# Performance work log

Hardware: AMD Instinct MI355X
Metric: run time of the kernel (lower is better)

## Reference

```python
import jax, jax.numpy as jnp
import numpy as np

E = 512   # embed_size == head_dim
H = 8     # heads
N = 8     # batch
S = 1024  # seq len


def setup_inputs() -> dict:
    key = jax.random.key(0)
    ks = jax.random.split(key, 12)
    scale = 1.0 / np.sqrt(E)
    inp = {
        "values": jax.random.normal(ks[0], (N, S, E), jnp.float32),
        "keys": jax.random.normal(ks[1], (N, S, E), jnp.float32),
        "query": jax.random.normal(ks[2], (N, S, E), jnp.float32),
        "pos": jnp.arange(S, dtype=jnp.int64) if jax.config.jax_enable_x64 else jnp.arange(S, dtype=jnp.int32),
        "mask": jax.random.randint(ks[3], (N, 1, S, S), 0, 2, jnp.int32),
        # nn.Linear params: weight (out,in), y = x @ W.T + b
        "Wv": jax.random.uniform(ks[4], (E * H, E), jnp.float32, -scale, scale),
        "bv": jax.random.uniform(ks[5], (E * H,), jnp.float32, -scale, scale),
        "Wk": jax.random.uniform(ks[6], (E * H, E), jnp.float32, -scale, scale),
        "bk": jax.random.uniform(ks[7], (E * H,), jnp.float32, -scale, scale),
        "Wq": jax.random.uniform(ks[8], (E * H, E), jnp.float32, -scale, scale),
        "bq": jax.random.uniform(ks[9], (E * H,), jnp.float32, -scale, scale),
        "Wo": jax.random.uniform(ks[10], (E, E), jnp.float32, -scale, scale),
        "bo": jax.random.uniform(ks[11], (E,), jnp.float32, -scale, scale),
    }
    return inp


def reference(values, keys, query, pos, mask, Wv, bv, Wk, bk, Wq, bq, Wo, bo):
    n, q_len, e = query.shape
    v_len = values.shape[1]
    k_len = keys.shape[1]
    h = Wq.shape[0] // e
    # QKV projections: E -> E*H, reshape to (N, L, H, E)
    v = (values @ Wv.T + bv).reshape(n, v_len, h, e)
    k = (keys @ Wk.T + bk).reshape(n, k_len, h, e)
    q = (query @ Wq.T + bq).reshape(n, q_len, h, e)
    # bilinear energy, no softmax
    energy = jnp.einsum('nqhd,nkhd->nhqk', q, k)
    energy = jnp.where(mask == 0, jnp.zeros((), energy.dtype), energy)
    attention = energy / jnp.asarray(e ** 0.5, energy.dtype)
    out = jnp.einsum('nhql,nlhd->nqhd', attention, v).sum(axis=2)  # sum over heads
    return out @ Wo.T + bo
```

## Files before the change

kernel.cpp:

```cpp
#include <hip/hip_runtime.h>


#define RS 0.04419417382415922f

typedef __attribute__((ext_vector_type(8))) short bf16x8;
typedef __attribute__((ext_vector_type(4))) float f32x4;

__device__ __forceinline__ unsigned short f2b(float f) {
  unsigned u = __builtin_bit_cast(unsigned, f);
  unsigned r = (u + 0x7FFFu + ((u >> 16) & 1u)) >> 16;
  return (unsigned short)r;
}
__device__ __forceinline__ float b2f(unsigned short h) {
  return __builtin_bit_cast(float, ((unsigned)h) << 16);
}

__global__ void k_fill(float* p, int n, float v) {
  int i = blockIdx.x * blockDim.x + threadIdx.x;
  int stride = gridDim.x * blockDim.x;
  for (; i < n; i += stride) p[i] = v;
}

__global__ void k_maskbits(const int* __restrict__ m,
                           unsigned* __restrict__ bits) {
  int wi = blockIdx.x * 256 + threadIdx.x;
  const int* src = m + (size_t)wi * 32;
  unsigned b = 0;
#pragma unroll
  for (int i = 0; i < 32; ++i) b |= (src[i] != 0 ? 1u : 0u) << i;
  bits[wi] = b;
}

__global__ void k_conv3(const float4* __restrict__ v,
                        const float4* __restrict__ k,
                        const float4* __restrict__ q, ushort4* __restrict__ d,
                        int n4, int dstride) {
  const float4* s = (blockIdx.z == 0) ? v : (blockIdx.z == 1) ? k : q;
  ushort4* dz = d + (size_t)blockIdx.z * dstride;
  int stride = gridDim.x * blockDim.x;
  for (int i = blockIdx.x * blockDim.x + threadIdx.x; i < n4; i += stride) {
    float4 x = s[i];
    ushort4 o;
    o.x = f2b(x.x); o.y = f2b(x.y); o.z = f2b(x.z); o.w = f2b(x.w);
    dz[i] = o;
  }
}

__global__ void k_convw(const float4* __restrict__ s, ushort4* __restrict__ d,
                        int n4, float scale) {
  int stride = gridDim.x * blockDim.x;
  for (int i = blockIdx.x * blockDim.x + threadIdx.x; i < n4; i += stride) {
    float4 v = s[i];
    ushort4 o;
    o.x = f2b(v.x * scale); o.y = f2b(v.y * scale);
    o.z = f2b(v.z * scale); o.w = f2b(v.w * scale);
    d[i] = o;
  }
}

__global__ void k_reduce(const unsigned short* __restrict__ a,
                         unsigned short* __restrict__ o, int total) {
  int i = blockIdx.x * blockDim.x + threadIdx.x;
  if (i >= total) return;
  int nl = i >> 17, j = i & 131071;
  const ushort4* av = (const ushort4*)a + (size_t)nl * 1048576;
  float4 s = {0.f, 0.f, 0.f, 0.f};
#pragma unroll
  for (int h = 0; h < 8; ++h) {
    ushort4 v = av[h * 131072 + j];
    s.x += b2f(v.x); s.y += b2f(v.y); s.z += b2f(v.z); s.w += b2f(v.w);
  }
  ushort4 r;
  r.x = f2b(s.x); r.y = f2b(s.y); r.z = f2b(s.z); r.w = f2b(s.w);
  ((ushort4*)o)[i] = r;
}

#define GLD16(gp, sp)                                              \
  __builtin_amdgcn_global_load_lds(                                \
      (const __attribute__((address_space(1))) void*)(gp),         \
      (__attribute__((address_space(3))) void*)(sp), 16, 0, 0)

template <int MODE>
__global__ __launch_bounds__(256) void k_gemm(
    const unsigned short* __restrict__ A, const unsigned short* __restrict__ B,
    const float* __restrict__ bi0, const float* __restrict__ bi1,
    const float* __restrict__ bi2, const unsigned* __restrict__ mbits,
    unsigned short* __restrict__ outb, float* __restrict__ outf, int n0,
    int xstr, int ostr) {
  __shared__ short smem[17408];
  char* const sb = (char*)smem;

  const int tid = threadIdx.x;
  const int wid = tid >> 6;
  const int lane = tid & 63;
  const int wr = wid >> 1, wc = wid & 1;
  const int l15 = lane & 15, l4 = lane >> 4;

  int bx, by, bz;
  if constexpr (MODE == 2 || MODE == 4) {
    bz = blockIdx.x; bx = blockIdx.y; by = blockIdx.z;
  } else {
    bx = blockIdx.x; by = blockIdx.y; bz = blockIdx.z;
  }

  constexpr int KSEG = (MODE == 4) ? 1024 : 512;
  constexpr int NK = KSEG / 32;

  f32x4 acc[4][4];
#pragma unroll
  for (int i = 0; i < 4; ++i)
#pragma unroll
    for (int j = 0; j < 4; ++j) acc[i][j] = (f32x4){0.f, 0.f, 0.f, 0.f};

  const unsigned short* Ab;
  const unsigned short* Bb;
  if constexpr (MODE == 5) {
    Ab = A + (size_t)bx * 128 * 512;
    Bb = B + (size_t)by * 128 * 512;
  } else if constexpr (MODE == 6) {
    Ab = A + (size_t)bz * xstr + (size_t)bx * 128 * 512;
    Bb = B + (size_t)bz * 2097152 + (size_t)by * 128 * 512;
  } else if constexpr (MODE == 2) {
    Ab = A + (size_t)bz * 524288 + (size_t)bx * 128 * 512;
    Bb = B + (size_t)bz * 524288 + (size_t)by * 128 * 512;
  } else {
    Ab = A + (size_t)bz * 1048576 + (size_t)bx * 128 * 1024;
    Bb = B + (size_t)bz * 524288 + (size_t)by * 128 * 1024;
  }

#define STAGE(buf, kc)                                             \
  {                                                                \
    _Pragma("unroll") for (int is = 0; is < 2; ++is) {             \
      int c = is * 256 + tid;                                      \
      int row = c >> 2, col = (c & 3) << 3;                        \
      GLD16(Ab + (size_t)row * KSEG + (kc)*32 + col,               \
            sb + (buf)*8192 + is * 4096 + wid * 1024);             \
      GLD16(Bb + (size_t)row * KSEG + (kc)*32 + col,               \
            sb + 16384 + (buf)*8192 + is * 4096 + wid * 1024);     \
    }                                                              \
  }

  STAGE(0, 0);
  int cur = 0;
#pragma unroll 4
  for (int kc = 0; kc < NK; ++kc) {
    __syncthreads();
    if (kc + 1 < NK) STAGE(cur ^ 1, kc + 1);
    bf16x8 af[4], bf_[4];
#pragma unroll
    for (int f = 0; f < 4; ++f) {
      af[f] = *(const bf16x8*)(sb + cur * 8192 +
                               ((wr * 64 + f * 16 + l15) << 6) + (l4 << 4));
      bf_[f] = *(const bf16x8*)(sb + 16384 + cur * 8192 +
                                ((wc * 64 + f * 16 + l15) << 6) + (l4 << 4));
    }
#pragma unroll
    for (int mf = 0; mf < 4; ++mf)
#pragma unroll
      for (int nf = 0; nf < 4; ++nf)
        acc[mf][nf] = __builtin_amdgcn_mfma_f32_16x16x32_bf16(
            af[mf], bf_[nf], acc[mf][nf], 0, 0, 0);
    cur ^= 1;
  }
#undef STAGE

  const int r0 = l4 * 4;
  const int c0 = l15;

  if constexpr (MODE != 5) {
    const bool transp = (MODE == 6) && (bz == 0);
    const float* bias =
        (MODE == 6) ? ((bz == 0) ? bi0 : (bz == 1) ? bi1 : bi2) : nullptr;
    const float bscale = (MODE == 6 && bz == 2) ? RS : 1.0f;
    __syncthreads();
#pragma unroll
    for (int nf = 0; nf < 4; ++nf) {
      int c_loc = wc * 64 + nf * 16 + c0;
      int c_ = by * 128 + c_loc;
      float bvl = (MODE == 6) ? bias[c_] * bscale : 0.f;
#pragma unroll
      for (int mf = 0; mf < 4; ++mf) {
#pragma unroll
        for (int r = 0; r < 4; ++r) {
          int r_loc = wr * 64 + mf * 16 + r0 + r;
          float v = acc[mf][nf][r] + bvl;
          unsigned short bb;
          if constexpr (MODE == 2) {
            int r_ = bx * 128 + r_loc;
            unsigned mw = mbits[((size_t)(n0 + (bz >> 3)) * 1024 + r_) * 32 +
                                (c_ >> 5)];
            bb = ((mw >> (c_ & 31)) & 1u) ? f2b(v) : (unsigned short)0;
          } else {
            bb = f2b(v);
          }
          if (transp)
            smem[c_loc * 136 + r_loc] = (short)bb;
          else
            smem[r_loc * 136 + c_loc] = (short)bb;
        }
      }
    }
    __syncthreads();
#pragma unroll
    for (int ch = 0; ch < 8; ++ch) {
      int idx = ch * 256 + tid;
      int row = idx >> 4;
      int col = (idx & 15) << 3;
      bf16x8 v = *(const bf16x8*)(smem + row * 136 + col);
      if constexpr (MODE == 2) {
        int r_ = bx * 128 + row, cB = by * 128 + col;
        *(bf16x8*)(outb + (size_t)bz * 1048576 + (size_t)r_ * 1024 + cB) = v;
      } else if constexpr (MODE == 4) {
        int r_ = bx * 128 + row, cB = by * 128 + col;
        *(bf16x8*)(outb + (size_t)bz * 524288 + (size_t)r_ * 512 + cB) = v;
      } else {
        unsigned short* O = outb + (size_t)bz * ostr;
        if (bz == 0) {
          int eB = by * 128 + row;
          int r_ = bx * 128 + col;
          int nl = r_ >> 10, s = r_ & 1023, h = eB >> 9, e = eB & 511;
          *(bf16x8*)(O + (((size_t)nl * 8 + h) * 512 + e) * 1024 + s) = v;
        } else {
          int r_ = bx * 128 + row, cB = by * 128 + col;
          int nl = r_ >> 10, s = r_ & 1023, h = cB >> 9, e = cB & 511;
          *(bf16x8*)(O + (((size_t)nl * 8 + h) * 1024 + s) * 512 + e) = v;
        }
      }
    }
  } else {
    float* const Cs32 = (float*)smem;
#pragma unroll
    for (int hh = 0; hh < 2; ++hh) {
      __syncthreads();
      if (wr == hh) {
#pragma unroll
        for (int nf = 0; nf < 4; ++nf) {
          int c_loc = wc * 64 + nf * 16 + c0;
          float bvl = bi0[by * 128 + c_loc];
#pragma unroll
          for (int mf = 0; mf < 4; ++mf)
#pragma unroll
            for (int r = 0; r < 4; ++r)
              Cs32[(mf * 16 + r0 + r) * 136 + c_loc] = acc[mf][nf][r] + bvl;
        }
      }
      __syncthreads();
#pragma unroll
      for (int ch = 0; ch < 8; ++ch) {
        int idx = ch * 256 + tid;
        int row = idx >> 5;
        int col = (idx & 31) << 2;
        float4 v = *(const float4*)(Cs32 + row * 136 + col);
        *(float4*)(outf + (size_t)(bx * 128 + hh * 64 + row) * 512 +
                   by * 128 + col) = v;
      }
    }
  }
}

extern "C" void kernel_launch(void* const* d_in, const int* in_sizes, int n_in,
                              void* d_out, int out_size, void* d_ws,
                              size_t ws_size, hipStream_t stream) {
  const float* values = (const float*)d_in[0];
  const float* keys = (const float*)d_in[1];
  const float* query = (const float*)d_in[2];
  const int* maskI = (const int*)d_in[4];
  const float* Wv = (const float*)d_in[5];
  const float* bv = (const float*)d_in[6];
  const float* Wk = (const float*)d_in[7];
  const float* bk = (const float*)d_in[8];
  const float* Wq = (const float*)d_in[9];
  const float* bq = (const float*)d_in[10];
  const float* Wo = (const float*)d_in[11];
  const float* bo = (const float*)d_in[12];
  float* dout = (float*)d_out;

  const int exp_sizes[13] = {4194304, 4194304, 4194304, 1024, 8388608,
                             2097152, 4096,    2097152, 4096, 2097152,
                             4096,    262144,  512};
  bool ok = (n_in == 13);
  if (ok)
    for (int i = 0; i < 13; ++i)
      if (in_sizes[i] != exp_sizes[i]) ok = false;
  if (!ok) {
    k_fill<<<512, 256, 0, stream>>>(dout, out_size, 1000.f);
    return;
  }

  const size_t SZT2 = 16777216, SZT4 = 33554432;
  const size_t need2 = 22544384 + 3 * SZT2 + 2 * SZT2;
  const size_t need4 = 22544384 + 3 * SZT4 + 2 * SZT4;
  const int NL = (ws_size >= need4) ? 4 : 2;
  if (ws_size < need2) {
    k_fill<<<512, 256, 0, stream>>>(dout, out_size, 2000.f);
    return;
  }
  const size_t SZT = (size_t)NL * 8388608;

  char* w = (char*)d_ws;
  unsigned short* Wvb = (unsigned short*)(w);
  unsigned short* Wob = (unsigned short*)(w + 12582912);
  unsigned short* Atb = (unsigned short*)(w + 13107200);
  unsigned* mbits = (unsigned*)(w + 21495808);
  unsigned short* VTb = (unsigned short*)(w + 22544384);
  unsigned short* Kb = (unsigned short*)(w + 22544384 + SZT);
  unsigned short* Qb = (unsigned short*)(w + 22544384 + 2 * SZT);
  unsigned short* Pb = (unsigned short*)(w + 22544384 + 3 * SZT);
  unsigned short* Xc = (unsigned short*)Pb;
  unsigned short* Ahb = (unsigned short*)Qb;

  k_convw<<<512, 256, 0, stream>>>((const float4*)Wv, (ushort4*)Wvb, 524288,
                                   1.0f);
  k_convw<<<512, 256, 0, stream>>>((const float4*)Wk, (ushort4*)(Wvb + 2097152),
                                   524288, 1.0f);
  k_convw<<<512, 256, 0, stream>>>((const float4*)Wq, (ushort4*)(Wvb + 4194304),
                                   524288, RS);
  k_convw<<<256, 256, 0, stream>>>((const float4*)Wo, (ushort4*)Wob, 65536,
                                   1.0f);
  k_maskbits<<<1024, 256, 0, stream>>>(maskI, mbits);

  const int xstr = NL * 524288;
  const int ostr = NL * 4194304;

  for (int it = 0; it < 8 / NL; ++it) {
    const int n0 = it * NL;
    const size_t xoff = (size_t)n0 * 524288;
    k_conv3<<<dim3(512 * NL, 1, 3), 256, 0, stream>>>(
        (const float4*)(values + xoff), (const float4*)(keys + xoff),
        (const float4*)(query + xoff), (ushort4*)Xc, NL * 131072, NL * 131072);
    k_gemm<6><<<dim3(NL * 8, 32, 3), 256, 0, stream>>>(
        Xc, Wvb, bv, bk, bq, nullptr, VTb, nullptr, 0, xstr, ostr);
    k_gemm<2><<<dim3(NL * 8, 8, 8), 256, 0, stream>>>(
        Qb, Kb, nullptr, nullptr, nullptr, mbits, Pb, nullptr, n0, 0, 0);
    k_gemm<4><<<dim3(NL * 8, 8, 4), 256, 0, stream>>>(
        Pb, VTb, nullptr, nullptr, nullptr, nullptr, Ahb, nullptr, 0, 0, 0);
    k_reduce<<<NL * 512, 256, 0, stream>>>(Ahb, Atb + (size_t)n0 * 524288,
                                           NL * 131072);
  }

  k_gemm<5><<<dim3(64, 4, 1), 256, 0, stream>>>(
      Atb, Wob, bo, nullptr, nullptr, nullptr, nullptr, dout, 0, 0, 0);
}
```

Before: 507.5 us.

## Accumulate four heads per block in P·V GEMM and remap QKV block order

The P·V GEMM now loops over four heads inside one block and keeps a single accumulator, so each block writes a partial sum over four heads. The head-sum reduction then only adds two partials instead of eight, which cuts bf16 intermediate traffic. The QKV projection GEMM also remaps its linear block id so consecutive blocks are spread across eight chunks, likely to balance work across XCDs or improve cache locality. In exchange the P·V grid has four times fewer blocks, which may lower occupancy and parallelism.

```diff
diff --git a/kernel.cpp b/kernel.cpp
--- a/kernel.cpp
+++ b/kernel.cpp
@@ -58,20 +58,18 @@
   }
 }
 
-__global__ void k_reduce(const unsigned short* __restrict__ a,
-                         unsigned short* __restrict__ o, int total) {
+__global__ void k_reduce2(const unsigned short* __restrict__ a,
+                          unsigned short* __restrict__ o, int total) {
   int i = blockIdx.x * blockDim.x + threadIdx.x;
   if (i >= total) return;
   int nl = i >> 17, j = i & 131071;
-  const ushort4* av = (const ushort4*)a + (size_t)nl * 1048576;
-  float4 s = {0.f, 0.f, 0.f, 0.f};
-#pragma unroll
-  for (int h = 0; h < 8; ++h) {
-    ushort4 v = av[h * 131072 + j];
-    s.x += b2f(v.x); s.y += b2f(v.y); s.z += b2f(v.z); s.w += b2f(v.w);
-  }
+  const ushort4* av = (const ushort4*)a + (size_t)nl * 262144;
+  ushort4 v0 = av[j], v1 = av[131072 + j];
   ushort4 r;
-  r.x = f2b(s.x); r.y = f2b(s.y); r.z = f2b(s.z); r.w = f2b(s.w);
+  r.x = f2b(b2f(v0.x) + b2f(v1.x));
+  r.y = f2b(b2f(v0.y) + b2f(v1.y));
+  r.z = f2b(b2f(v0.z) + b2f(v1.z));
+  r.w = f2b(b2f(v0.w) + b2f(v1.w));
   ((ushort4*)o)[i] = r;
 }
 
@@ -99,12 +97,23 @@
   int bx, by, bz;
   if constexpr (MODE == 2 || MODE == 4) {
     bz = blockIdx.x; bx = blockIdx.y; by = blockIdx.z;
+  } else if constexpr (MODE == 6) {
+    int gx = gridDim.x, gy = gridDim.y;
+    int lid = blockIdx.x + gx * (blockIdx.y + gy * blockIdx.z);
+    int total = gx * gy * gridDim.z;
+    int chunk = total >> 3;
+    int wg = (lid & 7) * chunk + (lid >> 3);
+    bx = wg % gx;
+    int t = wg / gx;
+    by = t % gy;
+    bz = t / gy;
   } else {
     bx = blockIdx.x; by = blockIdx.y; bz = blockIdx.z;
   }
 
   constexpr int KSEG = (MODE == 4) ? 1024 : 512;
   constexpr int NK = KSEG / 32;
+  constexpr int NSEG = (MODE == 4) ? 4 : 1;
 
   f32x4 acc[4][4];
 #pragma unroll
@@ -114,19 +123,6 @@
 
   const unsigned short* Ab;
   const unsigned short* Bb;
-  if constexpr (MODE == 5) {
-    Ab = A + (size_t)bx * 128 * 512;
-    Bb = B + (size_t)by * 128 * 512;
-  } else if constexpr (MODE == 6) {
-    Ab = A + (size_t)bz * xstr + (size_t)bx * 128 * 512;
-    Bb = B + (size_t)bz * 2097152 + (size_t)by * 128 * 512;
-  } else if constexpr (MODE == 2) {
-    Ab = A + (size_t)bz * 524288 + (size_t)bx * 128 * 512;
-    Bb = B + (size_t)bz * 524288 + (size_t)by * 128 * 512;
-  } else {
-    Ab = A + (size_t)bz * 1048576 + (size_t)bx * 128 * 1024;
-    Bb = B + (size_t)bz * 524288 + (size_t)by * 128 * 1024;
-  }
 
 #define STAGE(buf, kc)                                             \
   {                                                                \
@@ -140,27 +136,46 @@
     }                                                              \
   }
 
-  STAGE(0, 0);
-  int cur = 0;
+  for (int seg = 0; seg < NSEG; ++seg) {
+    if constexpr (MODE == 5) {
+      Ab = A + (size_t)bx * 128 * 512;
+      Bb = B + (size_t)by * 128 * 512;
+    } else if constexpr (MODE == 6) {
+      Ab = A + (size_t)bz * xstr + (size_t)bx * 128 * 512;
+      Bb = B + (size_t)bz * 2097152 + (size_t)by * 128 * 512;
+    } else if constexpr (MODE == 2) {
+      Ab = A + (size_t)bz * 524288 + (size_t)bx * 128 * 512;
+      Bb = B + (size_t)bz * 524288 + (size_t)by * 128 * 512;
+    } else {
+      int n_l = bz >> 1, g = bz & 1;
+      int nh = n_l * 8 + g * 4 + seg;
+      Ab = A + (size_t)nh * 1048576 + (size_t)bx * 128 * 1024;
+      Bb = B + (size_t)nh * 524288 + (size_t)by * 128 * 1024;
+    }
+
+    if (NSEG > 1 && seg > 0) __syncthreads();
+    STAGE(0, 0);
+    int cur = 0;
 #pragma unroll 4
-  for (int kc = 0; kc < NK; ++kc) {
-    __syncthreads();
-    if (kc + 1 < NK) STAGE(cur ^ 1, kc + 1);
-    bf16x8 af[4], bf_[4];
-#pragma unroll
-    for (int f = 0; f < 4; ++f) {
-      af[f] = *(const bf16x8*)(sb + cur * 8192 +
-                               ((wr * 64 + f * 16 + l15) << 6) + (l4 << 4));
-      bf_[f] = *(const bf16x8*)(sb + 16384 + cur * 8192 +
-                                ((wc * 64 + f * 16 + l15) << 6) + (l4 << 4));
-    }
-#pragma unroll
-    for (int mf = 0; mf < 4; ++mf)
-#pragma unroll
-      for (int nf = 0; nf < 4; ++nf)
-        acc[mf][nf] = __builtin_amdgcn_mfma_f32_16x16x32_bf16(
-            af[mf], bf_[nf], acc[mf][nf], 0, 0, 0);
-    cur ^= 1;
+    for (int kc = 0; kc < NK; ++kc) {
+      __syncthreads();
+      if (kc + 1 < NK) STAGE(cur ^ 1, kc + 1);
+      bf16x8 af[4], bf_[4];
+#pragma unroll
+      for (int f = 0; f < 4; ++f) {
+        af[f] = *(const bf16x8*)(sb + cur * 8192 +
+                                 ((wr * 64 + f * 16 + l15) << 6) + (l4 << 4));
+        bf_[f] = *(const bf16x8*)(sb + 16384 + cur * 8192 +
+                                  ((wc * 64 + f * 16 + l15) << 6) + (l4 << 4));
+      }
+#pragma unroll
+      for (int mf = 0; mf < 4; ++mf)
+#pragma unroll
+        for (int nf = 0; nf < 4; ++nf)
+          acc[mf][nf] = __builtin_amdgcn_mfma_f32_16x16x32_bf16(
+              af[mf], bf_[nf], acc[mf][nf], 0, 0, 0);
+      cur ^= 1;
+    }
   }
 #undef STAGE
 
@@ -332,10 +347,10 @@
         Xc, Wvb, bv, bk, bq, nullptr, VTb, nullptr, 0, xstr, ostr);
     k_gemm<2><<<dim3(NL * 8, 8, 8), 256, 0, stream>>>(
         Qb, Kb, nullptr, nullptr, nullptr, mbits, Pb, nullptr, n0, 0, 0);
-    k_gemm<4><<<dim3(NL * 8, 8, 4), 256, 0, stream>>>(
+    k_gemm<4><<<dim3(NL * 2, 8, 4), 256, 0, stream>>>(
         Pb, VTb, nullptr, nullptr, nullptr, nullptr, Ahb, nullptr, 0, 0, 0);
-    k_reduce<<<NL * 512, 256, 0, stream>>>(Ahb, Atb + (size_t)n0 * 524288,
-                                           NL * 131072);
+    k_reduce2<<<NL * 512, 256, 0, stream>>>(Ahb, Atb + (size_t)n0 * 524288,
+                                            NL * 131072);
   }
 
   k_gemm<5><<<dim3(64, 4, 1), 256, 0, stream>>>(
```

Measured after the change: 537.3 us. 1.06x slower.
